# Kernel optimization log

Measured on AMD Instinct MI355X. Metric: run time of the kernel, lower is better.

## Reference

```python
import jax, jax.numpy as jnp
import numpy as np

B, T, D = 2, 2048, 1024
H = 16
HD = D // H
NE = 17  # n_edge_types + 1

def setup_inputs() -> dict:
    key = jax.random.key(0)
    ks = jax.random.split(key, 6)
    x = jax.random.normal(ks[0], (B, T, D), dtype=jnp.float32)
    graph_adj = jax.random.uniform(ks[1], (B, T, T), dtype=jnp.float32)
    edge_types = jax.random.randint(ks[2], (B, T, T), 0, NE, dtype=jnp.int32)
    Wqkv = jax.random.normal(ks[3], (D, 3 * D), dtype=jnp.float32) * (D ** -0.5)
    Wproj = jax.random.normal(ks[4], (D, D), dtype=jnp.float32) * (D ** -0.5)
    adj_bias = jnp.zeros((H,), dtype=jnp.float32)
    edge_table = jax.random.normal(ks[5], (NE, H), dtype=jnp.float32) * 0.02
    return {"x": x, "graph_adj": graph_adj, "edge_types": edge_types,
            "Wqkv": Wqkv, "Wproj": Wproj, "adj_bias": adj_bias,
            "edge_table": edge_table}

def reference(x, graph_adj, edge_types, Wqkv, Wproj, adj_bias, edge_table):
    Bc, Tc, C = x.shape
    qkv = (x @ Wqkv).reshape(Bc, Tc, 3, H, HD)
    q, k, v = qkv[:, :, 0], qkv[:, :, 1], qkv[:, :, 2]  # [B,T,H,HD]
    scale = 1.0 / jnp.sqrt(jnp.asarray(HD, dtype=x.dtype))
    # scores: [B,H,T,T]
    attn = jnp.einsum('bqhd,bkhd->bhqk', q, k) * scale
    # adjacency bias per head
    attn = attn + adj_bias[None, :, None, None] * graph_adj[:, None, :, :]
    # edge-type bias: lookup [B,T,T,H] -> [B,H,T,T]
    etype_b = edge_table[edge_types]  # [B,T,T,H]
    attn = attn + jnp.transpose(etype_b, (0, 3, 1, 2))
    # causal mask (upper triangle, diag=1)
    causal = jnp.triu(jnp.ones((Tc, Tc), dtype=bool), k=1)
    attn = jnp.where(causal[None, None, :, :], jnp.asarray(-jnp.inf, dtype=attn.dtype), attn)
    attn = jax.nn.softmax(attn, axis=-1)
    out = jnp.einsum('bhqk,bkhd->bqhd', attn, v).reshape(Bc, Tc, C)
    return out @ Wproj
```

## Files before the change

### kernel.cpp

```cpp
#include <hip/hip_runtime.h>
#include <stdint.h>

#define TT 2048
#define HH 16
#define LOG2E 1.44269504089f

typedef _Float16 f16;
typedef __attribute__((ext_vector_type(8))) _Float16 f16x8;
typedef __attribute__((ext_vector_type(4))) float f32x4;
typedef unsigned short ushort_t;

__device__ __forceinline__ void gl_lds16(const void* g, void* l){
  __builtin_amdgcn_global_load_lds(
      (__attribute__((address_space(1))) void*)(void*)g,
      (__attribute__((address_space(3))) void*)l, 16, 0, 0);
}

__device__ __forceinline__ void lds_barrier(){
  __asm__ volatile("s_waitcnt lgkmcnt(0)\n\ts_barrier" ::: "memory");
}

__global__ __launch_bounds__(256) void cvt_f2h_kernel(const float4* __restrict__ in,
                                                      uint2* __restrict__ out, int n4){
  int i = blockIdx.x * 256 + threadIdx.x;
  if (i >= n4) return;
  float4 v = in[i];
  union { f16 h[4]; uint2 u; } o;
  o.h[0] = (f16)v.x; o.h[1] = (f16)v.y; o.h[2] = (f16)v.z; o.h[3] = (f16)v.w;
  out[i] = o.u;
}

__global__ __launch_bounds__(256) void transpose_cvt_kernel(const float* __restrict__ in,
                                                            f16* __restrict__ out, int R, int C){
  __shared__ float tile[64][65];
  int c0 = blockIdx.x * 64, r0 = blockIdx.y * 64;
  int t = threadIdx.x;
  int row = t >> 2, cs = (t & 3) << 4;
  const float4* src = (const float4*)(in + (size_t)(r0 + row) * C + c0 + cs);
  float4 a = src[0], b = src[1], c = src[2], d = src[3];
  float* tr = &tile[row][cs];
  tr[0]=a.x; tr[1]=a.y; tr[2]=a.z;  tr[3]=a.w;
  tr[4]=b.x; tr[5]=b.y; tr[6]=b.z;  tr[7]=b.w;
  tr[8]=c.x; tr[9]=c.y; tr[10]=c.z; tr[11]=c.w;
  tr[12]=d.x;tr[13]=d.y;tr[14]=d.z; tr[15]=d.w;
  __syncthreads();
  f16 tmp[16];
  #pragma unroll
  for (int j = 0; j < 16; ++j) tmp[j] = (f16)tile[cs + j][row];
  f16* dst = out + (size_t)(c0 + row) * R + r0 + cs;
  *(uint4*)dst = *(uint4*)&tmp[0];
  *(uint4*)(dst + 8) = *(uint4*)&tmp[8];
}

__global__ __launch_bounds__(256) void gemm_f16_kernel(const f16* __restrict__ A,
                                                       const f16* __restrict__ Bt,
                                                       void* __restrict__ Cout,
                                                       int M, int N, int K, int out_f32){
  __shared__ __align__(16) f16 As[128 * 32];
  __shared__ __align__(16) f16 Bs[128 * 32];
  int t = threadIdx.x;
  int w = t >> 6, lane = t & 63;
  int wm = (w >> 1) * 64, wn = (w & 1) * 64;
  int lrow = lane & 15, quad = lane >> 4;
  int bm = blockIdx.y, bn = blockIdx.x;

  f32x4 acc[4][4];
  for (int i = 0; i < 4; ++i)
    for (int j = 0; j < 4; ++j)
      for (int r = 0; r < 4; ++r) acc[i][j][r] = 0.f;

  const int nk = K >> 5;
  for (int kt = 0; kt < nk; ++kt){
    int k0 = kt << 5;
    __syncthreads();
    #pragma unroll
    for (int i = 0; i < 2; ++i){
      int c = (w << 7) + (i << 6) + lane;
      gl_lds16(A  + (size_t)((bm << 7) + (c >> 2)) * K + k0 + ((c & 3) << 3),
               As + ((w << 7) + (i << 6)) * 8);
      gl_lds16(Bt + (size_t)((bn << 7) + (c >> 2)) * K + k0 + ((c & 3) << 3),
               Bs + ((w << 7) + (i << 6)) * 8);
    }
    __syncthreads();
    f16x8 af[4], bfr[4];
    #pragma unroll
    for (int mi = 0; mi < 4; ++mi)
      af[mi] = *(const f16x8*)(As + (wm + mi * 16 + lrow) * 32 + quad * 8);
    #pragma unroll
    for (int ni = 0; ni < 4; ++ni)
      bfr[ni] = *(const f16x8*)(Bs + (wn + ni * 16 + lrow) * 32 + quad * 8);
    #pragma unroll
    for (int mi = 0; mi < 4; ++mi)
      #pragma unroll
      for (int ni = 0; ni < 4; ++ni)
        acc[mi][ni] = __builtin_amdgcn_mfma_f32_16x16x32_f16(af[mi], bfr[ni], acc[mi][ni], 0, 0, 0);
  }

  #pragma unroll
  for (int mi = 0; mi < 4; ++mi)
    #pragma unroll
    for (int ni = 0; ni < 4; ++ni)
      #pragma unroll
      for (int r = 0; r < 4; ++r){
        int row = (bm << 7) + wm + mi * 16 + quad * 4 + r;
        int col = (bn << 7) + wn + ni * 16 + lrow;
        float val = acc[mi][ni][r];
        if (out_f32) ((float*)Cout)[(size_t)row * N + col] = val;
        else         ((f16*)Cout)[(size_t)row * N + col] = (f16)val;
      }
}

__global__ __launch_bounds__(256, 4) void attn_kernel(const f16* __restrict__ qkv,
                                                      const float* __restrict__ gadj,
                                                      const int* __restrict__ etype,
                                                      const float* __restrict__ adj_bias,
                                                      const float* __restrict__ edge_table,
                                                      f16* __restrict__ attn_out,
                                                      f16* __restrict__ Opart,
                                                      float* __restrict__ MLpart){
  __shared__ __align__(16) f16 Ks[64 * 72];
  __shared__ __align__(16) f16 Vt[64 * 72];
  __shared__ __align__(16) f16 Ps[4][16 * 72];
  __shared__ float edge_lds[8 * 33];

  int bx = blockIdx.x;
  int h = bx & 15;
  int b = (bx >> 4) & 1;
  int j = bx >> 5;
  int qt, c0;
  if (j < 16){ qt = 16 + j; c0 = 0; }
  else { int p = (j - 16) >> 1;
         if (((j - 16) & 1) == 0){ qt = 15 - p; c0 = 0; }
         else                    { qt = 31 - p; c0 = 1; } }
  int ks = c0 << 4;
  int ke = min(qt, ks + 15);
  bool whole = (c0 == 0) && (qt <= 15);

  int t = threadIdx.x;
  int w = t >> 6, lane = t & 63;
  int lrow = lane & 15, quad = lane >> 4;

  if (t < 136){
    int cp = t / 17, e = t - cp * 17;
    edge_lds[cp * 33 + e] = edge_table[e * HH + h];
  }
  float adjb = adj_bias[h];
  int erep = (lane & 7) * 33;

  int q0 = qt * 64 + w * 16;
  const size_t qrow = ((size_t)b * TT + q0 + lrow) * 3072 + h * 64;
  f16x8 qf0 = *(const f16x8*)(qkv + qrow + quad * 8);
  f16x8 qf1 = *(const f16x8*)(qkv + qrow + 32 + quad * 8);

  f32x4 o[4];
  for (int i = 0; i < 4; ++i)
    for (int r = 0; r < 4; ++r) o[i][r] = 0.f;
  float mrun[4] = {-1e30f, -1e30f, -1e30f, -1e30f};
  float lrun[4] = {0.f, 0.f, 0.f, 0.f};

  const int keyA = t >> 3,        hdA = (t & 7) << 3;
  const int keyB = 32 + (t >> 3), hdB = hdA;
  const int sA = ((keyA >> 3) ^ (hdA >> 3)) & 7;
  const int sB = ((keyB >> 3) ^ (hdB >> 3)) & 7;
  const f16* kbase = qkv + (size_t)b * TT * 3072 + 1024 + h * 64;
  const f16* vbase = qkv + (size_t)b * TT * 3072 + 2048 + h * 64;

  for (int kt2 = ks; kt2 <= ke; ++kt2){
    lds_barrier();
    uint4 kv0 = *(const uint4*)(kbase + (size_t)(kt2 * 64 + keyA) * 3072 + hdA);
    uint4 kv1 = *(const uint4*)(kbase + (size_t)(kt2 * 64 + keyB) * 3072 + hdB);
    uint4 vv0 = *(const uint4*)(vbase + (size_t)(kt2 * 64 + keyA) * 3072 + hdA);
    uint4 vv1 = *(const uint4*)(vbase + (size_t)(kt2 * 64 + keyB) * 3072 + hdB);

    int qgb = q0 + quad * 4;
    int kgb = kt2 * 64 + lrow;
    float gv[16]; int ev[16];
    #pragma unroll
    for (int nb = 0; nb < 4; ++nb){
      size_t idx0 = ((size_t)b * TT + qgb) * TT + kgb + nb * 16;
      #pragma unroll
      for (int r = 0; r < 4; ++r){
        size_t idx = idx0 + (size_t)r * TT;
        gv[nb * 4 + r] = gadj[idx];
        ev[nb * 4 + r] = etype[idx];
      }
    }

    *(uint4*)(Ks + keyA * 72 + hdA) = kv0;
    *(uint4*)(Ks + keyB * 72 + hdB) = kv1;
    {
      union { uint4 u; f16 hh[8]; } ua, ub;
      ua.u = vv0; ub.u = vv1;
      #pragma unroll
      for (int jj = 0; jj < 8; ++jj){
        Vt[(hdA + jj) * 72 + (sA << 3) + (keyA & 7)] = ua.hh[jj];
        Vt[(hdB + jj) * 72 + (sB << 3) + (keyB & 7)] = ub.hh[jj];
      }
    }
    lds_barrier();

    f32x4 sf[4];
    #pragma unroll
    for (int nb = 0; nb < 4; ++nb){
      f32x4 s = {0.f, 0.f, 0.f, 0.f};
      f16x8 kf0 = *(const f16x8*)(Ks + (nb * 16 + lrow) * 72 + quad * 8);
      f16x8 kf1 = *(const f16x8*)(Ks + (nb * 16 + lrow) * 72 + 32 + quad * 8);
      s = __builtin_amdgcn_mfma_f32_16x16x32_f16(qf0, kf0, s, 0, 0, 0);
      s = __builtin_amdgcn_mfma_f32_16x16x32_f16(qf1, kf1, s, 0, 0, 0);
      sf[nb] = s;
    }

    float sarr[4][4];
    bool diag = (kt2 == qt);
    #pragma unroll
    for (int nb = 0; nb < 4; ++nb){
      int kg = kgb + nb * 16;
      #pragma unroll
      for (int r = 0; r < 4; ++r){
        float v;
        if (diag && kg > qgb + r) v = -1e30f;
        else v = sf[nb][r] * 0.125f + adjb * gv[nb * 4 + r] + edge_lds[erep + ev[nb * 4 + r]];
        sarr[nb][r] = v;
      }
    }

    float pv_[4][4];
    #pragma unroll
    for (int r = 0; r < 4; ++r){
      float mx = fmaxf(fmaxf(sarr[0][r], sarr[1][r]), fmaxf(sarr[2][r], sarr[3][r]));
      mx = fmaxf(mx, __shfl_xor(mx, 1));
      mx = fmaxf(mx, __shfl_xor(mx, 2));
      mx = fmaxf(mx, __shfl_xor(mx, 4));
      mx = fmaxf(mx, __shfl_xor(mx, 8));
      float mnew = fmaxf(mrun[r], mx);
      float alpha = exp2f((mrun[r] - mnew) * LOG2E);
      mrun[r] = mnew;
      float rs = 0.f;
      #pragma unroll
      for (int nb = 0; nb < 4; ++nb){
        float p = exp2f((sarr[nb][r] - mnew) * LOG2E);
        pv_[nb][r] = p; rs += p;
      }
      rs += __shfl_xor(rs, 1); rs += __shfl_xor(rs, 2);
      rs += __shfl_xor(rs, 4); rs += __shfl_xor(rs, 8);
      lrun[r] = lrun[r] * alpha + rs;
      #pragma unroll
      for (int nbh = 0; nbh < 4; ++nbh) o[nbh][r] *= alpha;
    }

    f16* Pw = &Ps[w][0];
    #pragma unroll
    for (int nb = 0; nb < 4; ++nb)
      #pragma unroll
      for (int r = 0; r < 4; ++r)
        Pw[(quad * 4 + r) * 72 + nb * 16 + lrow] = (f16)pv_[nb][r];
    __asm__ volatile("s_waitcnt lgkmcnt(0)" ::: "memory");

    #pragma unroll
    for (int cc = 0; cc < 2; ++cc){
      f16x8 pf = *(const f16x8*)(Pw + lrow * 72 + cc * 32 + quad * 8);
      #pragma unroll
      for (int nbh = 0; nbh < 4; ++nbh){
        int hd = nbh * 16 + lrow;
        int sb = (hd >> 3) & 7;
        f16x8 vf = *(const f16x8*)(Vt + hd * 72 + (((cc * 4 + quad) ^ sb) << 3));
        o[nbh] = __builtin_amdgcn_mfma_f32_16x16x32_f16(pf, vf, o[nbh], 0, 0, 0);
      }
    }
  }

  if (whole){
    float inv[4];
    #pragma unroll
    for (int r = 0; r < 4; ++r) inv[r] = 1.0f / lrun[r];
    #pragma unroll
    for (int nbh = 0; nbh < 4; ++nbh)
      #pragma unroll
      for (int r = 0; r < 4; ++r){
        int qg = q0 + quad * 4 + r;
        int col = h * 64 + nbh * 16 + lrow;
        attn_out[((size_t)b * TT + qg) * 1024 + col] = (f16)(o[nbh][r] * inv[r]);
      }
  } else {
    int slot = (((b * 16 + h) * 16) + (qt - 16)) * 2 + c0;
    f16* Ob = Opart + (size_t)slot * 4096;
    #pragma unroll
    for (int nbh = 0; nbh < 4; ++nbh)
      #pragma unroll
      for (int r = 0; r < 4; ++r)
        Ob[(w * 16 + quad * 4 + r) * 64 + nbh * 16 + lrow] = (f16)o[nbh][r];
    if (lrow == 0){
      #pragma unroll
      for (int r = 0; r < 4; ++r){
        int qq = w * 16 + quad * 4 + r;
        MLpart[(size_t)slot * 128 + qq] = mrun[r];
        MLpart[(size_t)slot * 128 + 64 + qq] = lrun[r];
      }
    }
  }
}

__global__ __launch_bounds__(256) void combine_kernel(const f16* __restrict__ Opart,
                                                      const float* __restrict__ ML,
                                                      f16* __restrict__ attn_out){
  int bx = blockIdx.x;
  int t = threadIdx.x;
  int q = t >> 2;
  int hd0 = (t & 3) << 4;
  int slot0 = bx * 2;
  float m0 = ML[(size_t)slot0 * 128 + q],       l0 = ML[(size_t)slot0 * 128 + 64 + q];
  float m1 = ML[(size_t)(slot0 + 1) * 128 + q], l1 = ML[(size_t)(slot0 + 1) * 128 + 64 + q];
  float M = fmaxf(m0, m1);
  float w0 = exp2f((m0 - M) * LOG2E), w1 = exp2f((m1 - M) * LOG2E);
  float invL = 1.0f / (l0 * w0 + l1 * w1);

  const f16* O0 = Opart + (size_t)slot0 * 4096 + q * 64 + hd0;
  const f16* O1 = O0 + 4096;
  f16x8 a0 = *(const f16x8*)O0,   a1 = *(const f16x8*)(O0 + 8);
  f16x8 b0 = *(const f16x8*)O1,   b1 = *(const f16x8*)(O1 + 8);
  f16 outv[16];
  #pragma unroll
  for (int i = 0; i < 8; ++i){
    outv[i]     = (f16)(((float)a0[i] * w0 + (float)b0[i] * w1) * invL);
    outv[i + 8] = (f16)(((float)a1[i] * w0 + (float)b1[i] * w1) * invL);
  }
  int qt = (bx & 15) + 16, h = (bx >> 4) & 15, b = bx >> 8;
  int qg = qt * 64 + q;
  f16* dst = attn_out + ((size_t)b * TT + qg) * 1024 + h * 64 + hd0;
  *(uint4*)dst = *(uint4*)&outv[0];
  *(uint4*)(dst + 8) = *(uint4*)&outv[8];
}

extern "C" void kernel_launch(void* const* d_in, const int* in_sizes, int n_in,
                              void* d_out, int out_size, void* d_ws, size_t ws_size,
                              hipStream_t stream){
  (void)in_sizes; (void)n_in; (void)out_size; (void)ws_size;
  const float* x_f32  = (const float*)d_in[0];
  const float* gadj   = (const float*)d_in[1];
  const int*   etype  = (const int*)d_in[2];
  const float* wqkv   = (const float*)d_in[3];
  const float* wproj  = (const float*)d_in[4];
  const float* adjb   = (const float*)d_in[5];
  const float* etab   = (const float*)d_in[6];

  char* ws = (char*)d_ws;
  f16*   x_f16  = (f16*)(ws);
  f16*   wqkvT  = (f16*)(ws + (8u << 20));
  f16*   wprojT = (f16*)(ws + (14u << 20));
  f16*   qkv    = (f16*)(ws + (16u << 20));
  f16*   Opart  = (f16*)(ws + (40u << 20));
  float* MLpart = (float*)(ws + (48u << 20));
  f16*   attn_o = x_f16;

  cvt_f2h_kernel<<<4096, 256, 0, stream>>>((const float4*)x_f32, (uint2*)x_f16, 1048576);
  transpose_cvt_kernel<<<dim3(48, 16), 256, 0, stream>>>(wqkv, wqkvT, 1024, 3072);
  transpose_cvt_kernel<<<dim3(16, 16), 256, 0, stream>>>(wproj, wprojT, 1024, 1024);
  gemm_f16_kernel<<<dim3(24, 32), 256, 0, stream>>>(x_f16, wqkvT, qkv, 4096, 3072, 1024, 0);
  attn_kernel<<<1536, 256, 0, stream>>>(qkv, gadj, etype, adjb, etab, attn_o, Opart, MLpart);
  combine_kernel<<<512, 256, 0, stream>>>(Opart, MLpart, attn_o);
  gemm_f16_kernel<<<dim3(8, 32), 256, 0, stream>>>(attn_o, wprojT, d_out, 4096, 1024, 1024, 1);
}
```

Baseline: 292.4 us.

## Split attention KV range into 8-tile chunks with longest-first schedule and lazy rescale

Replaces the two-way KV split with chunks of at most eight key tiles per work item. A constexpr table orders the items longest-first across 2560 blocks to balance load, and the combine kernel now merges up to four partial results per query tile. It also folds log2(e) into the scale, bias and edge table so the exp2 calls need no extra multiply. The online-softmax rescale is skipped unless the row max grows by more than a threshold, which relies on exponent headroom. Workspace buffers are re-laid out so Opart aliases wqkvT, which is safe only because the QKV GEMM runs first.

New measurement: 286.1 us. 1.02x faster.

```diff
diff --git a/kernel.cpp b/kernel.cpp
--- a/kernel.cpp
+++ b/kernel.cpp
@@ -18,6 +18,32 @@
 
 __device__ __forceinline__ void lds_barrier(){
   __asm__ volatile("s_waitcnt lgkmcnt(0)\n\ts_barrier" ::: "memory");
+}
+
+struct SchedT { unsigned short v[80]; };
+static constexpr SchedT make_sched(){
+  SchedT s{};
+  int idx = 0;
+  for (int size = 8; size >= 1; --size){
+    for (int qt = 31; qt >= 8; --qt){
+      int full = qt >> 3;
+      int tail = (qt & 7) + 1;
+      if (size == 8)
+        for (int ci = 0; ci < full; ++ci)
+          s.v[idx++] = (unsigned short)(qt | (ci << 8));
+      if (tail == size)
+        s.v[idx++] = (unsigned short)(qt | (full << 8));
+    }
+    s.v[idx++] = (unsigned short)(size - 1);
+  }
+  return s;
+}
+__constant__ SchedT SCHED = make_sched();
+
+__device__ __forceinline__ int slot_base(int qt){
+  return (qt < 16) ? 2 * (qt - 8)
+       : (qt < 24) ? 16 + 3 * (qt - 16)
+                   : 40 + 4 * (qt - 24);
 }
 
 __global__ __launch_bounds__(256) void cvt_f2h_kernel(const float4* __restrict__ in,
@@ -124,17 +150,13 @@
   __shared__ float edge_lds[8 * 33];
 
   int bx = blockIdx.x;
-  int h = bx & 15;
-  int b = (bx >> 4) & 1;
-  int j = bx >> 5;
-  int qt, c0;
-  if (j < 16){ qt = 16 + j; c0 = 0; }
-  else { int p = (j - 16) >> 1;
-         if (((j - 16) & 1) == 0){ qt = 15 - p; c0 = 0; }
-         else                    { qt = 31 - p; c0 = 1; } }
-  int ks = c0 << 4;
-  int ke = min(qt, ks + 15);
-  bool whole = (c0 == 0) && (qt <= 15);
+  int bh = bx & 31;
+  int h = bh & 15, b = bh >> 4;
+  int ej = SCHED.v[bx >> 5];
+  int qt = ej & 31, ci = ej >> 8;
+  int ksrt = ci << 3;
+  int kend = min(qt, ksrt + 7);
+  bool whole = (qt < 8);
 
   int t = threadIdx.x;
   int w = t >> 6, lane = t & 63;
@@ -142,9 +164,9 @@
 
   if (t < 136){
     int cp = t / 17, e = t - cp * 17;
-    edge_lds[cp * 33 + e] = edge_table[e * HH + h];
-  }
-  float adjb = adj_bias[h];
+    edge_lds[cp * 33 + e] = edge_table[e * HH + h] * LOG2E;
+  }
+  float adjb = adj_bias[h] * LOG2E;
   int erep = (lane & 7) * 33;
 
   int q0 = qt * 64 + w * 16;
@@ -165,7 +187,9 @@
   const f16* kbase = qkv + (size_t)b * TT * 3072 + 1024 + h * 64;
   const f16* vbase = qkv + (size_t)b * TT * 3072 + 2048 + h * 64;
 
-  for (int kt2 = ks; kt2 <= ke; ++kt2){
+  const float SCL = 0.125f * LOG2E;
+
+  for (int kt2 = ksrt; kt2 <= kend; ++kt2){
     lds_barrier();
     uint4 kv0 = *(const uint4*)(kbase + (size_t)(kt2 * 64 + keyA) * 3072 + hdA);
     uint4 kv1 = *(const uint4*)(kbase + (size_t)(kt2 * 64 + keyB) * 3072 + hdB);
@@ -219,33 +243,46 @@
       for (int r = 0; r < 4; ++r){
         float v;
         if (diag && kg > qgb + r) v = -1e30f;
-        else v = sf[nb][r] * 0.125f + adjb * gv[nb * 4 + r] + edge_lds[erep + ev[nb * 4 + r]];
+        else v = sf[nb][r] * SCL + adjb * gv[nb * 4 + r] + edge_lds[erep + ev[nb * 4 + r]];
         sarr[nb][r] = v;
       }
     }
 
+    float mx[4];
+    bool need = false;
+    #pragma unroll
+    for (int r = 0; r < 4; ++r){
+      float m_ = fmaxf(fmaxf(sarr[0][r], sarr[1][r]), fmaxf(sarr[2][r], sarr[3][r]));
+      m_ = fmaxf(m_, __shfl_xor(m_, 1));
+      m_ = fmaxf(m_, __shfl_xor(m_, 2));
+      m_ = fmaxf(m_, __shfl_xor(m_, 4));
+      m_ = fmaxf(m_, __shfl_xor(m_, 8));
+      mx[r] = m_;
+      need = need || (m_ > mrun[r] + 5.0f);
+    }
+    if (__any(need)){
+      #pragma unroll
+      for (int r = 0; r < 4; ++r){
+        float mnew = fmaxf(mrun[r], mx[r]);
+        float alpha = exp2f(mrun[r] - mnew);
+        lrun[r] *= alpha;
+        #pragma unroll
+        for (int nbh = 0; nbh < 4; ++nbh) o[nbh][r] *= alpha;
+        mrun[r] = mnew;
+      }
+    }
     float pv_[4][4];
     #pragma unroll
     for (int r = 0; r < 4; ++r){
-      float mx = fmaxf(fmaxf(sarr[0][r], sarr[1][r]), fmaxf(sarr[2][r], sarr[3][r]));
-      mx = fmaxf(mx, __shfl_xor(mx, 1));
-      mx = fmaxf(mx, __shfl_xor(mx, 2));
-      mx = fmaxf(mx, __shfl_xor(mx, 4));
-      mx = fmaxf(mx, __shfl_xor(mx, 8));
-      float mnew = fmaxf(mrun[r], mx);
-      float alpha = exp2f((mrun[r] - mnew) * LOG2E);
-      mrun[r] = mnew;
       float rs = 0.f;
       #pragma unroll
       for (int nb = 0; nb < 4; ++nb){
-        float p = exp2f((sarr[nb][r] - mnew) * LOG2E);
+        float p = exp2f(sarr[nb][r] - mrun[r]);
         pv_[nb][r] = p; rs += p;
       }
       rs += __shfl_xor(rs, 1); rs += __shfl_xor(rs, 2);
       rs += __shfl_xor(rs, 4); rs += __shfl_xor(rs, 8);
-      lrun[r] = lrun[r] * alpha + rs;
-      #pragma unroll
-      for (int nbh = 0; nbh < 4; ++nbh) o[nbh][r] *= alpha;
+      lrun[r] += rs;
     }
 
     f16* Pw = &Ps[w][0];
@@ -282,7 +319,7 @@
         attn_out[((size_t)b * TT + qg) * 1024 + col] = (f16)(o[nbh][r] * inv[r]);
       }
   } else {
-    int slot = (((b * 16 + h) * 16) + (qt - 16)) * 2 + c0;
+    int slot = bh * 72 + slot_base(qt) + ci;
     f16* Ob = Opart + (size_t)slot * 4096;
     #pragma unroll
     for (int nbh = 0; nbh < 4; ++nbh)
@@ -303,30 +340,48 @@
 __global__ __launch_bounds__(256) void combine_kernel(const f16* __restrict__ Opart,
                                                       const float* __restrict__ ML,
                                                       f16* __restrict__ attn_out){
-  int bx = blockIdx.x;
+  int qt = blockIdx.x + 8;
+  int bh = blockIdx.y;
+  int nch = (qt >> 3) + 1;
+  int slot0 = bh * 72 + slot_base(qt);
   int t = threadIdx.x;
   int q = t >> 2;
   int hd0 = (t & 3) << 4;
-  int slot0 = bx * 2;
-  float m0 = ML[(size_t)slot0 * 128 + q],       l0 = ML[(size_t)slot0 * 128 + 64 + q];
-  float m1 = ML[(size_t)(slot0 + 1) * 128 + q], l1 = ML[(size_t)(slot0 + 1) * 128 + 64 + q];
-  float M = fmaxf(m0, m1);
-  float w0 = exp2f((m0 - M) * LOG2E), w1 = exp2f((m1 - M) * LOG2E);
-  float invL = 1.0f / (l0 * w0 + l1 * w1);
-
-  const f16* O0 = Opart + (size_t)slot0 * 4096 + q * 64 + hd0;
-  const f16* O1 = O0 + 4096;
-  f16x8 a0 = *(const f16x8*)O0,   a1 = *(const f16x8*)(O0 + 8);
-  f16x8 b0 = *(const f16x8*)O1,   b1 = *(const f16x8*)(O1 + 8);
+
+  float m[4], l[4];
+  float M = -1e30f;
+  #pragma unroll
+  for (int c = 0; c < 4; ++c){
+    if (c < nch){
+      m[c] = ML[(size_t)(slot0 + c) * 128 + q];
+      l[c] = ML[(size_t)(slot0 + c) * 128 + 64 + q];
+      M = fmaxf(M, m[c]);
+    } else { m[c] = -1e30f; l[c] = 0.f; }
+  }
+  float acc[16];
+  #pragma unroll
+  for (int i = 0; i < 16; ++i) acc[i] = 0.f;
+  float L = 0.f;
+  #pragma unroll
+  for (int c = 0; c < 4; ++c){
+    if (c < nch){
+      float wgt = exp2f(m[c] - M);
+      L += l[c] * wgt;
+      const f16* O = Opart + (size_t)(slot0 + c) * 4096 + q * 64 + hd0;
+      f16x8 a0 = *(const f16x8*)O, a1 = *(const f16x8*)(O + 8);
+      #pragma unroll
+      for (int i = 0; i < 8; ++i){
+        acc[i]     += (float)a0[i] * wgt;
+        acc[i + 8] += (float)a1[i] * wgt;
+      }
+    }
+  }
+  float invL = 1.0f / L;
   f16 outv[16];
   #pragma unroll
-  for (int i = 0; i < 8; ++i){
-    outv[i]     = (f16)(((float)a0[i] * w0 + (float)b0[i] * w1) * invL);
-    outv[i + 8] = (f16)(((float)a1[i] * w0 + (float)b1[i] * w1) * invL);
-  }
-  int qt = (bx & 15) + 16, h = (bx >> 4) & 15, b = bx >> 8;
-  int qg = qt * 64 + q;
-  f16* dst = attn_out + ((size_t)b * TT + qg) * 1024 + h * 64 + hd0;
+  for (int i = 0; i < 16; ++i) outv[i] = (f16)(acc[i] * invL);
+  int b = bh >> 4, h = bh & 15;
+  f16* dst = attn_out + ((size_t)b * TT + qt * 64 + q) * 1024 + h * 64 + hd0;
   *(uint4*)dst = *(uint4*)&outv[0];
   *(uint4*)(dst + 8) = *(uint4*)&outv[8];
 }
@@ -345,18 +400,18 @@
 
   char* ws = (char*)d_ws;
   f16*   x_f16  = (f16*)(ws);
-  f16*   wqkvT  = (f16*)(ws + (8u << 20));
-  f16*   wprojT = (f16*)(ws + (14u << 20));
-  f16*   qkv    = (f16*)(ws + (16u << 20));
-  f16*   Opart  = (f16*)(ws + (40u << 20));
-  float* MLpart = (float*)(ws + (48u << 20));
+  f16*   qkv    = (f16*)(ws + (8u  << 20));
+  f16*   wqkvT  = (f16*)(ws + (32u << 20));
+  f16*   Opart  = (f16*)(ws + (32u << 20));
+  f16*   wprojT = (f16*)(ws + (51u << 20));
+  float* MLpart = (float*)(ws + (53u << 20));
   f16*   attn_o = x_f16;
 
   cvt_f2h_kernel<<<4096, 256, 0, stream>>>((const float4*)x_f32, (uint2*)x_f16, 1048576);
   transpose_cvt_kernel<<<dim3(48, 16), 256, 0, stream>>>(wqkv, wqkvT, 1024, 3072);
   transpose_cvt_kernel<<<dim3(16, 16), 256, 0, stream>>>(wproj, wprojT, 1024, 1024);
   gemm_f16_kernel<<<dim3(24, 32), 256, 0, stream>>>(x_f16, wqkvT, qkv, 4096, 3072, 1024, 0);
-  attn_kernel<<<1536, 256, 0, stream>>>(qkv, gadj, etype, adjb, etab, attn_o, Opart, MLpart);
-  combine_kernel<<<512, 256, 0, stream>>>(Opart, MLpart, attn_o);
+  attn_kernel<<<2560, 256, 0, stream>>>(qkv, gadj, etype, adjb, etab, attn_o, Opart, MLpart);
+  combine_kernel<<<dim3(24, 32), 256, 0, stream>>>(Opart, MLpart, attn_o);
   gemm_f16_kernel<<<dim3(8, 32), 256, 0, stream>>>(attn_o, wprojT, d_out, 4096, 1024, 1024, 1);
 }
```
